# Optimization experiments

Hardware: AMD Instinct MI355X
Metric: run time of the kernel (lower is better)

Reference implementation:

```python
import jax, jax.numpy as jnp
import numpy as np

B, T, C = 2, 2048, 2048
H, H_KV, D = 32, 8, 64
ROPE_THETA = 10000.0


def _rope_cos_sin(t, head_dim, theta=ROPE_THETA):
    # t: [T] positions. Returns interleaved cos/sin of shape [T, head_dim]
    inv_freq = 1.0 / theta ** (jnp.arange(0, head_dim, 2, dtype=jnp.float32) / head_dim)
    freqs = jnp.outer(t.astype(jnp.float32), inv_freq)  # [T, D/2]
    cos = jnp.stack([jnp.cos(freqs), jnp.cos(freqs)], axis=-1).reshape(t.shape[0], head_dim)
    sin = jnp.stack([jnp.sin(freqs), jnp.sin(freqs)], axis=-1).reshape(t.shape[0], head_dim)
    return cos[None, None], sin[None, None]  # [1,1,T,D]


def _rotate_half(x):
    half = x.shape[-1] // 2
    return jnp.concatenate([-x[..., half:], x[..., :half]], axis=-1)


def setup_inputs() -> dict:
    key = jax.random.key(0)
    ks = jax.random.split(key, 5)
    std = 0.02
    return {
        "x": jax.random.normal(ks[0], (B, T, C), dtype=jnp.float32),
        "Wq": jax.random.normal(ks[1], (H * D, C), dtype=jnp.float32) * std,
        "Wk": jax.random.normal(ks[2], (H_KV * D, C), dtype=jnp.float32) * std,
        "Wv": jax.random.normal(ks[3], (H_KV * D, C), dtype=jnp.float32) * std,
        "Wc": jax.random.normal(ks[4], (C, C), dtype=jnp.float32) * std,
        "position_ids": jnp.arange(T, dtype=jnp.int32)[None, :],  # [1, T]
    }


def reference(x, Wq, Wk, Wv, Wc, position_ids):
    b, t, c = x.shape
    # QKV projections (torch Linear: y = x @ W.T)
    q = (x @ Wq.T).reshape(b, t, H, D).transpose(0, 2, 1, 3)       # [B,H,T,D]
    k = (x @ Wk.T).reshape(b, t, H_KV, D).transpose(0, 2, 1, 3)    # [B,Hkv,T,D]
    v = (x @ Wv.T).reshape(b, t, H_KV, D).transpose(0, 2, 1, 3)
    # GQA expand: repeat_interleave along head dim
    rep = H // H_KV
    k = jnp.repeat(k, rep, axis=1)  # [B,H,T,D]
    v = jnp.repeat(v, rep, axis=1)
    # RoPE (single-batch branch: interleaved cos/sin)
    cos, sin = _rope_cos_sin(position_ids[0], D)
    q = q * cos + _rotate_half(q) * sin
    k = k * cos + _rotate_half(k) * sin
    # causal SDPA
    scale = 1.0 / jnp.sqrt(jnp.asarray(D, dtype=q.dtype))
    scores = jnp.einsum("bhqd,bhkd->bhqk", q, k) * scale
    causal = jnp.tril(jnp.ones((t, t), dtype=bool))
    scores = jnp.where(causal[None, None], scores, jnp.finfo(scores.dtype).min)
    attn = jax.nn.softmax(scores, axis=-1)
    y = jnp.einsum("bhqk,bhkd->bhqd", attn, v)  # [B,H,T,D]
    y = y.transpose(0, 2, 1, 3).reshape(b, t, c)
    return y @ Wc.T
```

## Files before the change

### kernel.cpp

```cpp
#include <hip/hip_runtime.h>

constexpr int B   = 2;
constexpr int T   = 2048;
constexpr int C   = 2048;
constexpr int H   = 32;
constexpr int HKV = 8;
constexpr int D   = 64;
constexpr float SCALE = 0.125f;

typedef __attribute__((ext_vector_type(8))) short bf16x8;
typedef __attribute__((ext_vector_type(4))) float f32x4;

__device__ __forceinline__ unsigned short f2bf(float f) {
    unsigned u = __builtin_bit_cast(unsigned, f);
    u += 0x7fff + ((u >> 16) & 1);
    return (unsigned short)(u >> 16);
}
__device__ __forceinline__ float bf2f(unsigned short u) {
    unsigned v = (unsigned)u << 16;
    return __builtin_bit_cast(float, v);
}
__device__ __forceinline__ unsigned cvt_pk_bf16(float lo, float hi) {
    unsigned r;
    asm("v_cvt_pk_bf16_f32 %0, %1, %2" : "=v"(r) : "v"(lo), "v"(hi));
    return r;
}

typedef __attribute__((address_space(1))) const unsigned char ga_t;
typedef __attribute__((address_space(3))) unsigned char lds_t;
__device__ __forceinline__ void gl2lds16(const void* g, void* l) {
    __builtin_amdgcn_global_load_lds((ga_t*)g, (lds_t*)l, 16, 0, 0);
}

__global__ __launch_bounds__(256) void cast_all_bf16(const float* __restrict__ x,
                                                     const float* __restrict__ wq,
                                                     const float* __restrict__ wk,
                                                     const float* __restrict__ wv,
                                                     const float* __restrict__ wc,
                                                     unsigned short* __restrict__ out) {
    const size_t b0 = (size_t)B * T * C;
    const size_t b1 = b0 + (size_t)H * D * C;
    const size_t b2 = b1 + (size_t)HKV * D * C;
    const size_t b3 = b2 + (size_t)HKV * D * C;
    size_t i = ((size_t)blockIdx.x * 256 + threadIdx.x) * 8;
    const float* src;
    size_t off;
    if (i < b0)      { src = x;  off = i; }
    else if (i < b1) { src = wq; off = i - b0; }
    else if (i < b2) { src = wk; off = i - b1; }
    else if (i < b3) { src = wv; off = i - b2; }
    else             { src = wc; off = i - b3; }
    float4 a = *(const float4*)(src + off);
    float4 b = *(const float4*)(src + off + 4);
    uint4 r;
    r.x = (unsigned)f2bf(a.x) | ((unsigned)f2bf(a.y) << 16);
    r.y = (unsigned)f2bf(a.z) | ((unsigned)f2bf(a.w) << 16);
    r.z = (unsigned)f2bf(b.x) | ((unsigned)f2bf(b.y) << 16);
    r.w = (unsigned)f2bf(b.z) | ((unsigned)f2bf(b.w) << 16);
    *(uint4*)(out + i) = r;
}

template <typename OutT>
__device__ __forceinline__ void gemm_mfma_body(const unsigned short* __restrict__ Xh,
                                               const unsigned short* __restrict__ Wh,
                                               OutT* __restrict__ Y,
                                               int Nloc, int K, int bm, int bn) {
    __shared__ __align__(16) unsigned short As[128 * 64];
    __shared__ __align__(16) unsigned short Bs[128 * 64];
    char* AsB = (char*)As;
    char* BsB = (char*)Bs;

    const int tid  = threadIdx.x;
    const int wave = tid >> 6, lane = tid & 63;
    const int wm = (wave >> 1) * 64, wn = (wave & 1) * 64;
    const int m = lane & 15, quad = lane >> 4;

    const int r0 = tid >> 3;
    const int cs = tid & 7;
    const int cg = cs ^ (r0 & 7);
    const int ldst = tid * 16;

    const unsigned short* gA = Xh + (size_t)(bm + r0) * K + cg * 8;
    const unsigned short* gB = Wh + (size_t)(bn + r0) * K + cg * 8;
    const size_t rowStep32 = (size_t)32 * K;

    int aoff[4][2], boff[4][2];
#pragma unroll
    for (int mt = 0; mt < 4; ++mt)
#pragma unroll
        for (int kk = 0; kk < 2; ++kk) {
            int ra = wm + mt * 16 + m;
            aoff[mt][kk] = ra * 128 + ((((kk * 4 + quad) ^ (ra & 7))) << 4);
            int rb = wn + mt * 16 + m;
            boff[mt][kk] = rb * 128 + ((((kk * 4 + quad) ^ (rb & 7))) << 4);
        }

    f32x4 acc[4][4];
#pragma unroll
    for (int i = 0; i < 4; ++i)
#pragma unroll
        for (int j = 0; j < 4; ++j) acc[i][j] = (f32x4){0.f, 0.f, 0.f, 0.f};

    for (int k0 = 0; k0 < K; k0 += 64) {
        gl2lds16(gA,                 AsB + ldst);
        gl2lds16(gA +     rowStep32, AsB +  4096 + ldst);
        gl2lds16(gA + 2 * rowStep32, AsB +  8192 + ldst);
        gl2lds16(gA + 3 * rowStep32, AsB + 12288 + ldst);
        gl2lds16(gB,                 BsB + ldst);
        gl2lds16(gB +     rowStep32, BsB +  4096 + ldst);
        gl2lds16(gB + 2 * rowStep32, BsB +  8192 + ldst);
        gl2lds16(gB + 3 * rowStep32, BsB + 12288 + ldst);
        gA += 64;
        gB += 64;
        __syncthreads();

#pragma unroll
        for (int kk = 0; kk < 2; ++kk) {
            bf16x8 af[4], bfr[4];
#pragma unroll
            for (int mt = 0; mt < 4; ++mt) af[mt]  = *(const bf16x8*)(AsB + aoff[mt][kk]);
#pragma unroll
            for (int nt = 0; nt < 4; ++nt) bfr[nt] = *(const bf16x8*)(BsB + boff[nt][kk]);
#pragma unroll
            for (int mt = 0; mt < 4; ++mt)
#pragma unroll
                for (int nt = 0; nt < 4; ++nt)
                    acc[mt][nt] = __builtin_amdgcn_mfma_f32_16x16x32_bf16(af[mt], bfr[nt],
                                                                          acc[mt][nt], 0, 0, 0);
        }
        __syncthreads();
    }

#pragma unroll
    for (int mt = 0; mt < 4; ++mt)
#pragma unroll
        for (int r = 0; r < 4; ++r) {
            size_t row = (size_t)(bm + wm + mt * 16 + quad * 4 + r);
#pragma unroll
            for (int nt = 0; nt < 4; ++nt) {
                int col = bn + wn + nt * 16 + m;
                float v = acc[mt][nt][r];
                if constexpr (sizeof(OutT) == 2)
                    Y[row * Nloc + col] = f2bf(v);
                else
                    Y[row * Nloc + col] = v;
            }
        }
}

__global__ __launch_bounds__(256) void qkv_gemm_bf16(const unsigned short* __restrict__ Xh,
                                                     const unsigned short* __restrict__ Wqh,
                                                     const unsigned short* __restrict__ Wkh,
                                                     const unsigned short* __restrict__ Wvh,
                                                     unsigned short* __restrict__ qh,
                                                     unsigned short* __restrict__ kh,
                                                     unsigned short* __restrict__ vh) {
    int bn0 = blockIdx.x * 128;
    const unsigned short* Wsel;
    unsigned short* Ysel;
    int bnl, Nloc;
    if (bn0 < H * D)                { Wsel = Wqh; Ysel = qh; bnl = bn0;                  Nloc = H * D;   }
    else if (bn0 < H*D + HKV*D)     { Wsel = Wkh; Ysel = kh; bnl = bn0 - H * D;          Nloc = HKV * D; }
    else                            { Wsel = Wvh; Ysel = vh; bnl = bn0 - H*D - HKV*D;    Nloc = HKV * D; }
    gemm_mfma_body<unsigned short>(Xh, Wsel, Ysel, Nloc, C, blockIdx.y * 128, bnl);
}

__global__ __launch_bounds__(256) void out_gemm_bf16(const unsigned short* __restrict__ Xh,
                                                     const unsigned short* __restrict__ Wh,
                                                     float* __restrict__ Y) {
    gemm_mfma_body<float>(Xh, Wh, Y, C, C, blockIdx.y * 128, blockIdx.x * 128);
}

__global__ void rope_fused(unsigned short* __restrict__ qh, unsigned short* __restrict__ kh,
                           const int* __restrict__ pos_ids, float qscale) {
    int idx = blockIdx.x * blockDim.x + threadIdx.x;
    const int qtotal = B * T * H * 32;
    unsigned short* buf;
    int nheads, rel;
    float sc;
    if (idx < qtotal) { buf = qh; nheads = H;   sc = qscale; rel = idx; }
    else              { buf = kh; nheads = HKV; sc = 1.0f;   rel = idx - qtotal; }
    int d = rel & 31;
    int rest = rel >> 5;
    int t = (rest / nheads) % T;
    float pos = (float)pos_ids[t];
    int i1 = d >> 1;
    const float NEG_LF = -(2.0f / 64.0f) * 13.287712379549449f;
    float a1 = pos * exp2f(NEG_LF * (float)i1);
    float a2 = pos * exp2f(NEG_LF * (float)(i1 + 16));
    float c1 = cosf(a1), s1 = sinf(a1);
    float c2 = cosf(a2), s2 = sinf(a2);
    size_t base = (size_t)rest * D + d;
    float x1 = bf2f(buf[base]), x2 = bf2f(buf[base + 32]);
    buf[base]      = f2bf((x1 * c1 - x2 * s1) * sc);
    buf[base + 32] = f2bf((x2 * c2 + x1 * s2) * sc);
}

__global__ __launch_bounds__(256) void v_transpose(const unsigned short* __restrict__ vh,
                                                   unsigned short* __restrict__ vtg) {
    __shared__ unsigned short Vs[64][72];
    const int t0 = blockIdx.x * 64;
    const int hkv = blockIdx.y;
    const int b = blockIdx.z;
    const int tid = threadIdx.x;

    for (int e = tid; e < 512; e += 256) {
        int t = e >> 3, d8 = (e & 7) * 8;
        uint4 val = *(const uint4*)(vh + ((size_t)((b * T + t0 + t) * HKV) + hkv) * D + d8);
        unsigned short tmp[8];
        *(uint4*)tmp = val;
#pragma unroll
        for (int i = 0; i < 8; ++i) Vs[d8 + i][t] = tmp[i];
    }
    __syncthreads();
    for (int e = tid; e < 512; e += 256) {
        int d = e >> 3, c = e & 7;
        *(uint4*)(vtg + ((size_t)((b * HKV + hkv) * D) + d) * T + t0 + c * 8) =
            *(const uint4*)&Vs[d][c * 8];
    }
}

__global__ __launch_bounds__(256, 4) void flash_attn_mfma(const unsigned short* __restrict__ Qh,
                                                          const unsigned short* __restrict__ Kh,
                                                          const unsigned short* __restrict__ Vtg,
                                                          unsigned short* __restrict__ Yh) {
    __shared__ __align__(16) unsigned short Ks[64 * 64];
    __shared__ __align__(16) unsigned short Vt[64 * 64];

    const int pairi = blockIdx.x;
    const int h  = blockIdx.y;
    const int b  = blockIdx.z;
    const int hkv = h >> 2;
    const int tid = threadIdx.x;
    const int wave = tid >> 6;
    const int lane = tid & 63;
    const int m = lane & 15;
    const int quad = lane >> 4;

    const int r0 = tid >> 3, cs = tid & 7, cg = cs ^ (r0 & 7);
    const int wbase = (tid & 192) * 16;
    char* KsB = (char*)Ks;
    char* VtB = (char*)Vt;

    const int m7 = m & 7;
    const int pwr = wave * 2048 + m * 128 + ((quad & 1) * 8);
    const int qh2 = quad >> 1;
    const int prd = wave * 2048 + m * 128;

    const unsigned short* gKbase = Kh + ((size_t)(b * T) * HKV + hkv) * D
                                      + (size_t)r0 * (HKV * D) + cg * 8;
    const unsigned short* gVbase = Vtg + ((size_t)(b * HKV + hkv) * D) * (size_t)T
                                       + (size_t)r0 * T + cg * 8;

#pragma unroll 1
    for (int half = 0; half < 2; ++half) {
        const int qt = half ? pairi : (T / 64 - 1 - pairi);
        const int q0 = qt * 64;
        const int qmin = q0 + wave * 16;

        const unsigned short* qrow = Qh + ((size_t)((b * T + q0 + wave * 16 + m) * H) + h) * D;
        const bf16x8 qa0 = *(const bf16x8*)(qrow + quad * 8);
        const bf16x8 qa1 = *(const bf16x8*)(qrow + 32 + quad * 8);

        f32x4 o[4];
#pragma unroll
        for (int dt = 0; dt < 4; ++dt) o[dt] = (f32x4){0.f, 0.f, 0.f, 0.f};
        float ms = -1e30f, ls = 0.f;

        const unsigned short* gK = gKbase;
        const unsigned short* gV = gVbase;

        for (int k0 = 0; k0 <= q0; k0 += 64) {
            gl2lds16(gK,                          KsB + wbase);
            gl2lds16(gK + (size_t)32 * (HKV * D), KsB + 4096 + wbase);
            gl2lds16(gV,                          VtB + wbase);
            gl2lds16(gV + (size_t)32 * T,         VtB + 4096 + wbase);
            gK += (size_t)64 * (HKV * D);
            gV += 64;
            __syncthreads();

            f32x4 s[4];
            __builtin_amdgcn_s_setprio(1);
#pragma unroll
            for (int nt = 0; nt < 4; ++nt) {
                const int kmin = k0 + nt * 16;
                if (kmin > qmin + 15) {
                    s[nt] = (f32x4){-1e30f, -1e30f, -1e30f, -1e30f};
                    continue;
                }
                int row = nt * 16 + m;
                const bf16x8 ka0 = *(const bf16x8*)(KsB + row * 128 + ((quad ^ (m & 7)) * 16));
                const bf16x8 ka1 = *(const bf16x8*)(KsB + row * 128 + (((quad + 4) ^ (m & 7)) * 16));
                f32x4 acc = (f32x4){0.f, 0.f, 0.f, 0.f};
                acc = __builtin_amdgcn_mfma_f32_16x16x32_bf16(ka0, qa0, acc, 0, 0, 0);
                acc = __builtin_amdgcn_mfma_f32_16x16x32_bf16(ka1, qa1, acc, 0, 0, 0);
                if (kmin + 15 > qmin) {
                    int c0 = qmin - kmin + m - 4 * quad;
#pragma unroll
                    for (int r = 0; r < 4; ++r)
                        if (r > c0) acc[r] = -1e30f;
                }
                s[nt] = acc;
            }
            __builtin_amdgcn_s_setprio(0);

            __syncthreads();

            float mx = s[0][0];
#pragma unroll
            for (int nt = 0; nt < 4; ++nt)
#pragma unroll
                for (int r = 0; r < 4; ++r) mx = fmaxf(mx, s[nt][r]);
            mx = fmaxf(mx, __shfl_xor(mx, 16));
            mx = fmaxf(mx, __shfl_xor(mx, 32));

            float al = 1.0f;
            if (__any(mx > ms + 8.0f)) {
                float mnew = fmaxf(ms, mx);
                al = exp2f(ms - mnew);
                ms = mnew;
                float av[4];
#pragma unroll
                for (int r = 0; r < 4; ++r)
                    av[r] = __shfl(al, quad * 20 + r);
#pragma unroll
                for (int dt = 0; dt < 4; ++dt)
#pragma unroll
                    for (int r = 0; r < 4; ++r) o[dt][r] *= av[r];
            }

            float psum = 0.f;
#pragma unroll
            for (int nt = 0; nt < 4; ++nt) {
                float p0 = exp2f(s[nt][0] - ms);
                float p1 = exp2f(s[nt][1] - ms);
                float p2 = exp2f(s[nt][2] - ms);
                float p3 = exp2f(s[nt][3] - ms);
                psum += (p0 + p1) + (p2 + p3);
                uint2 w;
                w.x = cvt_pk_bf16(p0, p1);
                w.y = cvt_pk_bf16(p2, p3);
                *(uint2*)(KsB + pwr + (((2 * nt + qh2) ^ m7) << 4)) = w;
            }
            psum += __shfl_xor(psum, 16);
            psum += __shfl_xor(psum, 32);
            ls = ls * al + psum;

            const bf16x8 pa0 = *(const bf16x8*)(KsB + prd + ((quad ^ m7) << 4));
            const bf16x8 pa1 = *(const bf16x8*)(KsB + prd + (((quad + 4) ^ m7) << 4));
            __builtin_amdgcn_s_setprio(1);
#pragma unroll
            for (int dt = 0; dt < 4; ++dt) {
                int vrow = dt * 16 + m;
                const bf16x8 vb0 = *(const bf16x8*)(VtB + vrow * 128 + ((quad ^ (m & 7)) * 16));
                const bf16x8 vb1 = *(const bf16x8*)(VtB + vrow * 128 + (((quad + 4) ^ (m & 7)) * 16));
                o[dt] = __builtin_amdgcn_mfma_f32_16x16x32_bf16(pa0, vb0, o[dt], 0, 0, 0);
                o[dt] = __builtin_amdgcn_mfma_f32_16x16x32_bf16(pa1, vb1, o[dt], 0, 0, 0);
            }
            __builtin_amdgcn_s_setprio(0);
            __syncthreads();
        }

#pragma unroll
        for (int r = 0; r < 4; ++r) {
            float lv = __shfl(ls, quad * 20 + r);
            float inv = 1.0f / lv;
            int trow = q0 + wave * 16 + quad * 4 + r;
            unsigned short* yp = Yh + ((size_t)(b * T + trow) * H + h) * D;
#pragma unroll
            for (int dt = 0; dt < 4; ++dt)
                yp[dt * 16 + m] = f2bf(o[dt][r] * inv);
        }
    }
}

extern "C" void kernel_launch(void* const* d_in, const int* in_sizes, int n_in,
                              void* d_out, int out_size, void* d_ws, size_t ws_size,
                              hipStream_t stream) {
    const float* x  = (const float*)d_in[0];
    const float* Wq = (const float*)d_in[1];
    const float* Wk = (const float*)d_in[2];
    const float* Wv = (const float*)d_in[3];
    const float* Wc = (const float*)d_in[4];
    const int*  pos = (const int*)d_in[5];
    float* out = (float*)d_out;

    unsigned short* xh  = (unsigned short*)d_ws;
    unsigned short* wqh = xh  + (size_t)B * T * C;
    unsigned short* wkh = wqh + (size_t)H * D * C;
    unsigned short* wvh = wkh + (size_t)HKV * D * C;
    unsigned short* wch = wvh + (size_t)HKV * D * C;
    unsigned short* qh  = wch + (size_t)C * C;
    unsigned short* kh  = qh  + (size_t)B * T * H * D;
    unsigned short* vh  = kh  + (size_t)B * T * HKV * D;
    unsigned short* vtg = vh  + (size_t)B * T * HKV * D;
    unsigned short* yh  = xh;

    const size_t cast_total = (size_t)B * T * C + (size_t)(H + 2 * HKV) * D * C + (size_t)C * C;
    cast_all_bf16<<<(unsigned)(cast_total / (256 * 8)), 256, 0, stream>>>(x, Wq, Wk, Wv, Wc, xh);

    dim3 g1((H * D + 2 * HKV * D) / 128, (B * T) / 128);
    qkv_gemm_bf16<<<g1, 256, 0, stream>>>(xh, wqh, wkh, wvh, qh, kh, vh);

    const float QSCALE = SCALE * 1.4426950408889634f;
    rope_fused<<<(B * T * (H + HKV) * 32) / 256, 256, 0, stream>>>(qh, kh, pos, QSCALE);
    v_transpose<<<dim3(T / 64, HKV, B), 256, 0, stream>>>(vh, vtg);

    dim3 g2(T / 128, H, B);
    flash_attn_mfma<<<g2, 256, 0, stream>>>(qh, kh, vtg, yh);

    dim3 g3(C / 128, (B * T) / 128);
    out_gemm_bf16<<<g3, 256, 0, stream>>>(yh, wch, out);
}
```

Baseline: 320.7 us.

## Double-buffer K/V tiles in LDS and prefetch the next tile during compute

Splits the K and V shared-memory tiles into two buffers. The first tile is loaded before the loop, and each iteration issues the global-to-LDS load for the next tile before the QK^T and PV math on the current one, so load latency overlaps with MFMA work. The mid-loop barrier becomes a raw s_barrier that waits only on LDS counters, leaving the prefetch loads in flight. The cost is double the LDS per block, which may limit occupancy, and correctness now depends on the end-of-loop sync draining the outstanding vector-memory loads.

```diff
diff --git a/kernel.cpp b/kernel.cpp
--- a/kernel.cpp
+++ b/kernel.cpp
@@ -224,8 +224,8 @@
                                                           const unsigned short* __restrict__ Kh,
                                                           const unsigned short* __restrict__ Vtg,
                                                           unsigned short* __restrict__ Yh) {
-    __shared__ __align__(16) unsigned short Ks[64 * 64];
-    __shared__ __align__(16) unsigned short Vt[64 * 64];
+    __shared__ __align__(16) unsigned short Ks[2][64 * 64];
+    __shared__ __align__(16) unsigned short Vt[2][64 * 64];
 
     const int pairi = blockIdx.x;
     const int h  = blockIdx.y;
@@ -251,6 +251,8 @@
                                       + (size_t)r0 * (HKV * D) + cg * 8;
     const unsigned short* gVbase = Vtg + ((size_t)(b * HKV + hkv) * D) * (size_t)T
                                        + (size_t)r0 * T + cg * 8;
+    const size_t kStep = (size_t)64 * (HKV * D);
+    const size_t kHalf = (size_t)32 * (HKV * D);
 
 #pragma unroll 1
     for (int half = 0; half < 2; ++half) {
@@ -270,14 +272,29 @@
         const unsigned short* gK = gKbase;
         const unsigned short* gV = gVbase;
 
+        gl2lds16(gK,         KsB + wbase);
+        gl2lds16(gK + kHalf, KsB + 4096 + wbase);
+        gl2lds16(gV,                  VtB + wbase);
+        gl2lds16(gV + (size_t)32 * T, VtB + 4096 + wbase);
+        gK += kStep;
+        gV += 64;
+        __syncthreads();
+
         for (int k0 = 0; k0 <= q0; k0 += 64) {
-            gl2lds16(gK,                          KsB + wbase);
-            gl2lds16(gK + (size_t)32 * (HKV * D), KsB + 4096 + wbase);
-            gl2lds16(gV,                          VtB + wbase);
-            gl2lds16(gV + (size_t)32 * T,         VtB + 4096 + wbase);
-            gK += (size_t)64 * (HKV * D);
-            gV += 64;
-            __syncthreads();
+            const int cur = (k0 >> 6) & 1;
+            char* KsC = KsB + cur * 8192;
+            char* VtC = VtB + cur * 8192;
+
+            if (k0 + 64 <= q0) {
+                char* KsN = KsB + (cur ^ 1) * 8192;
+                char* VtN = VtB + (cur ^ 1) * 8192;
+                gl2lds16(gK,         KsN + wbase);
+                gl2lds16(gK + kHalf, KsN + 4096 + wbase);
+                gl2lds16(gV,                  VtN + wbase);
+                gl2lds16(gV + (size_t)32 * T, VtN + 4096 + wbase);
+                gK += kStep;
+                gV += 64;
+            }
 
             f32x4 s[4];
             __builtin_amdgcn_s_setprio(1);
@@ -289,8 +306,8 @@
                     continue;
                 }
                 int row = nt * 16 + m;
-                const bf16x8 ka0 = *(const bf16x8*)(KsB + row * 128 + ((quad ^ (m & 7)) * 16));
-                const bf16x8 ka1 = *(const bf16x8*)(KsB + row * 128 + (((quad + 4) ^ (m & 7)) * 16));
+                const bf16x8 ka0 = *(const bf16x8*)(KsC + row * 128 + ((quad ^ (m & 7)) * 16));
+                const bf16x8 ka1 = *(const bf16x8*)(KsC + row * 128 + (((quad + 4) ^ (m & 7)) * 16));
                 f32x4 acc = (f32x4){0.f, 0.f, 0.f, 0.f};
                 acc = __builtin_amdgcn_mfma_f32_16x16x32_bf16(ka0, qa0, acc, 0, 0, 0);
                 acc = __builtin_amdgcn_mfma_f32_16x16x32_bf16(ka1, qa1, acc, 0, 0, 0);
@@ -304,7 +321,10 @@
             }
             __builtin_amdgcn_s_setprio(0);
 
-            __syncthreads();
+            __builtin_amdgcn_sched_barrier(0);
+            asm volatile("s_waitcnt lgkmcnt(0)" ::: "memory");
+            __builtin_amdgcn_s_barrier();
+            __builtin_amdgcn_sched_barrier(0);
 
             float mx = s[0][0];
 #pragma unroll
@@ -340,20 +360,20 @@
                 uint2 w;
                 w.x = cvt_pk_bf16(p0, p1);
                 w.y = cvt_pk_bf16(p2, p3);
-                *(uint2*)(KsB + pwr + (((2 * nt + qh2) ^ m7) << 4)) = w;
+                *(uint2*)(KsC + pwr + (((2 * nt + qh2) ^ m7) << 4)) = w;
             }
             psum += __shfl_xor(psum, 16);
             psum += __shfl_xor(psum, 32);
             ls = ls * al + psum;
 
-            const bf16x8 pa0 = *(const bf16x8*)(KsB + prd + ((quad ^ m7) << 4));
-            const bf16x8 pa1 = *(const bf16x8*)(KsB + prd + (((quad + 4) ^ m7) << 4));
+            const bf16x8 pa0 = *(const bf16x8*)(KsC + prd + ((quad ^ m7) << 4));
+            const bf16x8 pa1 = *(const bf16x8*)(KsC + prd + (((quad + 4) ^ m7) << 4));
             __builtin_amdgcn_s_setprio(1);
 #pragma unroll
             for (int dt = 0; dt < 4; ++dt) {
                 int vrow = dt * 16 + m;
-                const bf16x8 vb0 = *(const bf16x8*)(VtB + vrow * 128 + ((quad ^ (m & 7)) * 16));
-                const bf16x8 vb1 = *(const bf16x8*)(VtB + vrow * 128 + (((quad + 4) ^ (m & 7)) * 16));
+                const bf16x8 vb0 = *(const bf16x8*)(VtC + vrow * 128 + ((quad ^ (m & 7)) * 16));
+                const bf16x8 vb1 = *(const bf16x8*)(VtC + vrow * 128 + (((quad + 4) ^ (m & 7)) * 16));
                 o[dt] = __builtin_amdgcn_mfma_f32_16x16x32_bf16(pa0, vb0, o[dt], 0, 0, 0);
                 o[dt] = __builtin_amdgcn_mfma_f32_16x16x32_bf16(pa1, vb1, o[dt], 0, 0, 0);
             }
```

New measurement: 315.5 us. About the same (-1.6%).
